# Kernel tuning notes

Measured on AMD Instinct MI355X. Metric: run time of the kernel, lower is better.

## Reference

```python
import jax, jax.numpy as jnp
import numpy as np

EPSILON = 1e-06
MAXIMUM_AREA_RATIO = 0.3
GRID_HEIGHT = 160.0
CUBE = (25.0, 25.0, 32.0)
FEAT_SCALE = 1.0
GRID_SCALE = 1.0
CRANGE = (-1.0, 0.95)


def setup_inputs() -> dict:
    key = jax.random.key(0)
    k1, k2, k3, k4, k5 = jax.random.split(key, 5)
    B, C, H, W = 2, 256, 96, 320
    L, Wg = 128, 128
    n_layers = int(GRID_HEIGHT // CUBE[2])  # 5
    return {
        "feature": jax.random.normal(k1, (B, C, H, W), dtype=jnp.float32),
        "calib": jax.random.normal(k2, (B, 3, 4), dtype=jnp.float32),
        "grid": jax.random.normal(k3, (L, Wg, 3), dtype=jnp.float32),
        "Wc": jax.random.normal(k4, (C, C * n_layers), dtype=jnp.float32) * 0.02,
        "bc": jax.random.normal(k5, (C,), dtype=jnp.float32) * 0.02,
    }


def _cube_corners(cube):
    l, w, h = cube
    x = np.array([-l / 2, l / 2, l / 2, -l / 2, -l / 2, l / 2, l / 2, -l / 2])
    y = np.array([-w / 2, -w / 2, w / 2, w / 2, -w / 2, -w / 2, w / 2, w / 2])
    z = np.array([0, 0, 0, 0, h, h, h, h])
    return jnp.asarray(np.stack([x, y, z], axis=-1), dtype=jnp.float32)  # (8,3)


def _grid_sample_zeros(img, grd):
    # img: [B,C,H,W]; grd: [B,Hg,Wg,2] normalized coords in [-1,1]
    # bilinear, zero padding, align_corners=False (torch default)
    B, C, H, W = img.shape
    x = ((grd[..., 0] + 1.0) * W - 1.0) * 0.5
    y = ((grd[..., 1] + 1.0) * H - 1.0) * 0.5
    x0f = jnp.floor(x)
    y0f = jnp.floor(y)
    x0 = x0f.astype(jnp.int32)
    y0 = y0f.astype(jnp.int32)
    img_flat = img.reshape(B, C, H * W)

    def gather(xi, yi):
        valid = (xi >= 0) & (xi < W) & (yi >= 0) & (yi < H)
        xc = jnp.clip(xi, 0, W - 1)
        yc = jnp.clip(yi, 0, H - 1)
        idx = (yc * W + xc).reshape(B, 1, -1)
        v = jnp.take_along_axis(img_flat, idx, axis=2)
        v = v.reshape((B, C) + grd.shape[1:-1])
        return v * valid[:, None].astype(img.dtype)

    wx1 = x - x0f
    wx0 = 1.0 - wx1
    wy1 = y - y0f
    wy0 = 1.0 - wy1
    out = (gather(x0, y0) * (wx0 * wy0)[:, None]
           + gather(x0 + 1, y0) * (wx1 * wy0)[:, None]
           + gather(x0, y0 + 1) * (wx0 * wy1)[:, None]
           + gather(x0 + 1, y0 + 1) * (wx1 * wy1)[:, None])
    return out


def reference(feature, calib, grid, Wc, bc):
    B, C, H, W = feature.shape
    L, Wg, _ = grid.shape
    dtype = feature.dtype

    # z-layer offsets: (n_layers, 3) with offset only in z
    z_off = jnp.arange(0.0, GRID_HEIGHT, CUBE[2], dtype=dtype)  # (5,)
    n_layers = z_off.shape[0]
    z_corners = jnp.stack([jnp.zeros_like(z_off), jnp.zeros_like(z_off), z_off], axis=-1)
    offset = _cube_corners(CUBE)  # (8,3)

    # corners3d: (n_layers, L, Wg, 8, 3)
    corners = grid[None] + z_corners[:, None, None, :]  # (n,L,Wg,3)
    corners3d = (corners[:, :, :, None, :] + offset[None, None, None]) / GRID_SCALE

    # project with calib (B,3,4): homogeneous matmul then perspective divide
    hom = jnp.concatenate([corners3d, jnp.ones_like(corners3d[..., :1])], axis=-1)  # (n,L,Wg,8,4)
    pts = jnp.einsum('bij,nlwkj->bnlwki', calib, hom)  # (B,n,L,Wg,8,3)
    img_xy = pts[..., :2] / jnp.maximum(pts[..., 2:3], EPSILON)

    img_size = jnp.array([W, H], dtype=dtype) / FEAT_SCALE
    norm = jnp.clip(2.0 * img_xy / img_size - 1.0, CRANGE[0], CRANGE[1])  # (B,n,L,Wg,8,2)

    box_corners = jnp.concatenate([
        jnp.min(norm[..., 0], axis=-1, keepdims=True),
        jnp.min(norm[..., 1], axis=-1, keepdims=True),
        jnp.max(norm[..., 0], axis=-1, keepdims=True),
        jnp.max(norm[..., 1], axis=-1, keepdims=True),
    ], axis=-1)  # (B,n,L,Wg,4)
    box_corners = box_corners.reshape(B, n_layers, L * Wg, 4)

    area = ((box_corners[..., 2:] - box_corners[..., :2]).prod(axis=-1) * (H * W) + EPSILON)
    area = area[:, None]  # (B,1,n,LWg)
    visible = ((area > EPSILON) & (area < H * W * MAXIMUM_AREA_RATIO)).astype(dtype)

    integral = jnp.cumsum(jnp.cumsum(feature, axis=-1), axis=-2)

    lt = _grid_sample_zeros(integral, box_corners[..., [0, 1]])
    rb = _grid_sample_zeros(integral, box_corners[..., [2, 3]])
    rt = _grid_sample_zeros(integral, box_corners[..., [2, 1]])
    lb = _grid_sample_zeros(integral, box_corners[..., [0, 3]])

    vox = (lt + rb - rt - lb) / area * visible  # (B,C,n,LWg)
    # permute(0,3,1,2) -> (B, LWg, C, n); flatten to (B*LWg, C*n)
    vox = jnp.transpose(vox, (0, 3, 1, 2)).reshape(B * L * Wg, C * n_layers)

    ortho = vox @ Wc.T + bc  # (B*LWg, C)
    ortho = ortho.reshape(B, L, Wg, C)
    ortho = jax.nn.relu(jnp.transpose(ortho, (0, 3, 1, 2)))  # (B,C,L,Wg)
    return ortho
```

## Files before the change

### kernel.cpp

```cpp
#include <hip/hip_runtime.h>
#include <hip/hip_bf16.h>
#include <stdint.h>

#define BB 2
#define CC 256
#define HH 96
#define WW 320
#define NPIX 16384
#define NLAY 5
#define KDIM 1280
#define NDIM 32768
#define NKT (KDIM / 32)

typedef float f32x4 __attribute__((ext_vector_type(4)));
typedef float f32x2 __attribute__((ext_vector_type(2)));
typedef __bf16 bf16x8 __attribute__((ext_vector_type(8)));
typedef __bf16 bf16x4 __attribute__((ext_vector_type(4)));

__global__ __launch_bounds__(1024) void k1f(const float* __restrict__ feat,
                                            float* __restrict__ integ,
                                            const float* __restrict__ gridp,
                                            const float* __restrict__ calib,
                                            const float* __restrict__ Wc,
                                            float4* __restrict__ coords,
                                            float* __restrict__ scales,
                                            __bf16* __restrict__ Wbf) {
  const int bid = blockIdx.x;
  if (bid < 480) {
    const int vbid = bid * 4 + (threadIdx.x >> 8);
    const int vt = threadIdx.x & 255;
    if (vbid >= 640) {
      int o = (vbid - 640) * 256 + vt;
      int co = o / KDIM;
      int kk = o % KDIM;
      int n = kk >> 8;
      int c = kk & 255;
      Wbf[o] = (__bf16)Wc[co * KDIM + c * NLAY + n];
      return;
    }
    int box = vbid * 256 + vt;
    int pix = box & (NPIX - 1);
    int bn = box >> 14;
    int n = bn % NLAY;
    int b = bn / NLAY;
    const float* cb = calib + b * 12;
    float c00 = cb[0], c01 = cb[1], c02 = cb[2], c03 = cb[3];
    float c10 = cb[4], c11 = cb[5], c12 = cb[6], c13 = cb[7];
    float c20 = cb[8], c21 = cb[9], c22 = cb[10], c23 = cb[11];
    float gx = gridp[pix * 3 + 0], gy = gridp[pix * 3 + 1], gz = gridp[pix * 3 + 2];
    float zoff = 32.0f * (float)n;
    const float ox[8] = {-12.5f, 12.5f, 12.5f, -12.5f, -12.5f, 12.5f, 12.5f, -12.5f};
    const float oy[8] = {-12.5f, -12.5f, 12.5f, 12.5f, -12.5f, -12.5f, 12.5f, 12.5f};
    float xmn = 1e30f, ymn = 1e30f, xmx = -1e30f, ymx = -1e30f;
#pragma unroll
    for (int k = 0; k < 8; ++k) {
      float X = gx + ox[k];
      float Y = gy + oy[k];
      float Z = gz + zoff + ((k >= 4) ? 32.0f : 0.0f);
      float px = c00 * X + c01 * Y + c02 * Z + c03;
      float py = c10 * X + c11 * Y + c12 * Z + c13;
      float pz = c20 * X + c21 * Y + c22 * Z + c23;
      float d = fmaxf(pz, 1e-6f);
      float nx = fminf(fmaxf(2.0f * (px / d) / 320.0f - 1.0f, -1.0f), 0.95f);
      float ny = fminf(fmaxf(2.0f * (py / d) / 96.0f - 1.0f, -1.0f), 0.95f);
      xmn = fminf(xmn, nx); xmx = fmaxf(xmx, nx);
      ymn = fminf(ymn, ny); ymx = fmaxf(ymx, ny);
    }
    float dx = xmx - xmn, dy = ymx - ymn;
    float area = (dx * dy) * 30720.0f + 1e-6f;
    bool vis = (area > 1e-6f) && (area < 9216.0f);
    float X0 = ((xmn + 1.0f) * 320.0f - 1.0f) * 0.5f;
    float Y0 = ((ymn + 1.0f) * 96.0f - 1.0f) * 0.5f;
    float X1 = ((xmx + 1.0f) * 320.0f - 1.0f) * 0.5f;
    float Y1 = ((ymx + 1.0f) * 96.0f - 1.0f) * 0.5f;
    coords[box] = make_float4(X0, Y0, X1, Y1);
    scales[box] = vis ? 1.0f / area : 0.0f;
    return;
  }
  __shared__ float tile[WW * 33];
  const int t = threadIdx.x;
  const int wave = t >> 6;
  const int lane = t & 63;
  const int kb = bid - 480;
  const int cg = kb & 7;
  const int h = (kb >> 3) % HH;
  const int b = kb / (8 * HH);
  const int c0 = cg * 32;

  {
    const float* fb = feat + (size_t)((b * CC + c0) * HH + h) * WW;
    const size_t crstride = (size_t)HH * WW;
#pragma unroll
    for (int r = 0; r < 3; ++r) {
      int idx = r * 1024 + t;
      if (idx < 2560) {
        int cr = idx / 80;
        int wq = idx - cr * 80;
        f32x4 v = *(const f32x4*)(fb + cr * crstride + wq * 4);
        *(f32x4*)(&tile[cr * WW + wq * 4]) = v;
      }
    }
  }
  __syncthreads();
  const int ca = wave * 2, cbn = wave * 2 + 1;
  float va[5], vb[5];
#pragma unroll
  for (int j = 0; j < 5; ++j) va[j] = tile[ca * WW + lane * 5 + j];
#pragma unroll
  for (int j = 0; j < 5; ++j) vb[j] = tile[cbn * WW + lane * 5 + j];
#pragma unroll
  for (int j = 1; j < 5; ++j) { va[j] += va[j - 1]; vb[j] += vb[j - 1]; }
  float ta = va[4], tb = vb[4];
  float ia = ta, ib = tb;
#pragma unroll
  for (int d = 1; d < 64; d <<= 1) {
    float ua = __shfl_up(ia, d, 64);
    float ub = __shfl_up(ib, d, 64);
    if (lane >= d) { ia += ua; ib += ub; }
  }
  float pa = ia - ta, pb = ib - tb;
#pragma unroll
  for (int j = 0; j < 5; ++j) { va[j] += pa; vb[j] += pb; }
  __syncthreads();
#pragma unroll
  for (int j = 0; j < 5; ++j) {
    int w = lane * 5 + j;
    tile[w * 33 + ca]  = va[j];
    tile[w * 33 + cbn] = vb[j];
  }
  __syncthreads();
  float* dst = integ + (size_t)((b * HH + h) * WW) * CC + cg * 32;
#pragma unroll
  for (int r = 0; r < 3; ++r) {
    int idx = r * 1024 + t;
    if (idx < 2560) {
      int w = idx >> 3;
      int cq = (idx & 7) * 4;
      float4 o = make_float4(tile[w * 33 + cq + 0], tile[w * 33 + cq + 1],
                             tile[w * 33 + cq + 2], tile[w * 33 + cq + 3]);
      *(float4*)(dst + (size_t)w * CC + cq) = o;
    }
  }
}

__global__ __launch_bounds__(256) void k2_scan(float* __restrict__ integ) {
  const int blk = blockIdx.x;
  const int cq = blk & 1;
  const int w = (blk >> 1) % WW;
  const int b = blk / (2 * WW);
  const int g = threadIdx.x >> 6;
  const int l = threadIdx.x & 63;
  float* base = integ + ((size_t)(b * HH + g * 24) * WW + w) * CC + cq * 128 + l * 2;
  const size_t stride = (size_t)WW * CC;
  f32x2 v[24];
#pragma unroll
  for (int i = 0; i < 24; ++i) v[i] = *(const f32x2*)(base + (size_t)i * stride);
#pragma unroll
  for (int i = 1; i < 24; ++i) v[i] += v[i - 1];
  __shared__ f32x2 part[4][64];
  part[g][l] = v[23];
  __syncthreads();
  f32x2 off = {0.f, 0.f};
#pragma unroll
  for (int gg = 0; gg < 3; ++gg)
    if (gg < g) off += part[gg][l];
#pragma unroll
  for (int i = 0; i < 24; ++i) *(f32x2*)(base + (size_t)i * stride) = v[i] + off;
}

__global__ __launch_bounds__(256) void k4_vox(const float* __restrict__ integ,
                                              const float4* __restrict__ coords,
                                              const float* __restrict__ scales,
                                              __bf16* __restrict__ voxA) {
  const int wave = threadIdx.x >> 6;
  const int lane = threadIdx.x & 63;
  const int box0 = (blockIdx.x * 4 + wave) * 4;
#pragma unroll
  for (int u = 0; u < 4; ++u) {
    const int box = box0 + u;
    const int pix = box & (NPIX - 1);
    const int bn = box >> 14;
    const int n = bn % NLAY;
    const int b = bn / NLAY;
    const size_t row = (size_t)(b * NPIX + pix);
    bf16x4* dst = (bf16x4*)(voxA + row * KDIM + n * CC + lane * 4);
    const float scale = scales[box];
    if (scale == 0.f) {
      *dst = bf16x4{(__bf16)0.f, (__bf16)0.f, (__bf16)0.f, (__bf16)0.f};
      continue;
    }
    const float4 q = coords[box];

    float xw[4]; int xi[4];
    float yw[4]; int yi[4];
    {
      float f0 = floorf(q.x); int i0 = (int)f0; float w1 = q.x - f0;
      xw[0] = (i0 >= 0 && i0 < WW) ? (1.f - w1) : 0.f;
      xw[1] = (i0 + 1 < WW) ? w1 : 0.f;
      xi[0] = min(max(i0, 0), WW - 1); xi[1] = min(max(i0 + 1, 0), WW - 1);
      float f1 = floorf(q.z); int i1 = (int)f1; float v1 = q.z - f1;
      xw[2] = (i1 >= 0 && i1 < WW) ? -(1.f - v1) : 0.f;
      xw[3] = (i1 + 1 < WW) ? -v1 : 0.f;
      xi[2] = min(max(i1, 0), WW - 1); xi[3] = min(max(i1 + 1, 0), WW - 1);
    }
    {
      float f0 = floorf(q.y); int j0 = (int)f0; float w1 = q.y - f0;
      yw[0] = (j0 >= 0 && j0 < HH) ? (1.f - w1) : 0.f;
      yw[1] = (j0 + 1 < HH) ? w1 : 0.f;
      yi[0] = min(max(j0, 0), HH - 1); yi[1] = min(max(j0 + 1, 0), HH - 1);
      float f1 = floorf(q.w); int j1 = (int)f1; float v1 = q.w - f1;
      yw[2] = (j1 >= 0 && j1 < HH) ? -(1.f - v1) : 0.f;
      yw[3] = (j1 + 1 < HH) ? -v1 : 0.f;
      yi[2] = min(max(j1, 0), HH - 1); yi[3] = min(max(j1 + 1, 0), HH - 1);
    }
    const float* base = integ + (size_t)(b * HH) * WW * CC + lane * 4;
    f32x4 val = {0.f, 0.f, 0.f, 0.f};
#pragma unroll
    for (int jj = 0; jj < 4; ++jj) {
      if (yw[jj] == 0.f) continue;
      const float* rp = base + (size_t)yi[jj] * WW * CC;
      f32x4 rs = {0.f, 0.f, 0.f, 0.f};
#pragma unroll
      for (int ii = 0; ii < 4; ++ii) {
        if (xw[ii] != 0.f) {
          f32x4 v = *(const f32x4*)(rp + (size_t)xi[ii] * CC);
          rs += xw[ii] * v;
        }
      }
      val += yw[jj] * rs;
    }
    val *= scale;
    *dst = bf16x4{(__bf16)val.x, (__bf16)val.y, (__bf16)val.z, (__bf16)val.w};
  }
}

__device__ __forceinline__ void glds16(const void* g, void* l) {
  __builtin_amdgcn_global_load_lds(
      (const __attribute__((address_space(1))) void*)g,
      (__attribute__((address_space(3))) void*)(uint32_t)(uintptr_t)l,
      16, 0, 0);
}

__global__ __launch_bounds__(256) void k6_gemm(const __bf16* __restrict__ A,
                                               const __bf16* __restrict__ Bm,
                                               const float* __restrict__ bias,
                                               float* __restrict__ out) {
  __shared__ __align__(16) __bf16 As[4][128 * 32];
  __shared__ __align__(16) __bf16 Bs[4][128 * 32];
  const int tileM = blockIdx.y * 128;
  const int tileN = blockIdx.x * 128;
  const int tid = threadIdx.x;
  const int lane = tid & 63;
  const int wave = tid >> 6;
  const int wm = (wave >> 1) * 64;
  const int wn = (wave & 1) * 64;

  f32x4 acc[4][4];
#pragma unroll
  for (int i = 0; i < 4; ++i)
#pragma unroll
    for (int j = 0; j < 4; ++j)
      acc[i][j] = f32x4{0.f, 0.f, 0.f, 0.f};

  const int r16 = lane & 15;
  const int q4 = lane >> 4;
  const int srow = (lane >> 2);
  const int sch = lane & 3;

  auto stage = [&](int buf, int kt) {
    const int k0 = kt * 32;
#pragma unroll
    for (int rr = 0; rr < 2; ++rr) {
      const int base_row = wave * 16 + rr * 64;
      const int row = base_row + srow;
      const int gch = sch ^ ((row >> 1) & 3);
      glds16(A  + (size_t)(tileM + row) * KDIM + k0 + gch * 8,
             (void*)(&As[buf][base_row * 32] + lane * 8));
      glds16(Bm + (size_t)(tileN + row) * KDIM + k0 + gch * 8,
             (void*)(&Bs[buf][base_row * 32] + lane * 8));
    }
  };

  stage(0, 0);
  stage(1, 1);
  stage(2, 2);
  for (int kt = 0; kt < NKT; ++kt) {
    const int cur = kt & 3;
    if (kt < NKT - 2)       __builtin_amdgcn_s_waitcnt(0xF78);
    else if (kt == NKT - 2) __builtin_amdgcn_s_waitcnt(0xF74);
    else                    __builtin_amdgcn_s_waitcnt(0xF70);
    __builtin_amdgcn_s_barrier();
    if (kt + 3 < NKT) stage((kt + 3) & 3, kt + 3);
    bf16x8 af[4], bg[4];
#pragma unroll
    for (int i = 0; i < 4; ++i) {
      int m = wm + i * 16 + r16;
      af[i] = *(const bf16x8*)(&As[cur][m * 32] + (q4 ^ ((m >> 1) & 3)) * 8);
    }
#pragma unroll
    for (int j = 0; j < 4; ++j) {
      int nr = wn + j * 16 + r16;
      bg[j] = *(const bf16x8*)(&Bs[cur][nr * 32] + (q4 ^ ((nr >> 1) & 3)) * 8);
    }
#pragma unroll
    for (int i = 0; i < 4; ++i)
#pragma unroll
      for (int j = 0; j < 4; ++j)
        acc[i][j] = __builtin_amdgcn_mfma_f32_16x16x32_bf16(af[i], bg[j], acc[i][j], 0, 0, 0);
  }

#pragma unroll
  for (int i = 0; i < 4; ++i) {
#pragma unroll
    for (int j = 0; j < 4; ++j) {
      int nn = tileN + wn + j * 16 + r16;
      int bI = nn >> 14;
      int pix = nn & (NPIX - 1);
#pragma unroll
      for (int r = 0; r < 4; ++r) {
        int co = tileM + wm + i * 16 + q4 * 4 + r;
        float v = acc[i][j][r] + bias[co];
        out[(size_t)(bI * CC + co) * NPIX + pix] = fmaxf(v, 0.f);
      }
    }
  }
}

extern "C" void kernel_launch(void* const* d_in, const int* in_sizes, int n_in,
                              void* d_out, int out_size, void* d_ws, size_t ws_size,
                              hipStream_t stream) {
  const float* feat  = (const float*)d_in[0];
  const float* calib = (const float*)d_in[1];
  const float* grid  = (const float*)d_in[2];
  const float* Wc    = (const float*)d_in[3];
  const float* bc    = (const float*)d_in[4];
  float* out = (float*)d_out;

  char* ws = (char*)d_ws;
  const size_t SZ_INTEG = (size_t)BB * HH * WW * CC * 4;
  const size_t SZ_VOX   = (size_t)NDIM * KDIM * 2;
  const size_t SZ_WBF   = (size_t)CC * KDIM * 2;
  const size_t SZ_CRD   = (size_t)BB * NLAY * NPIX * 16;
  const size_t SZ_SCL   = (size_t)BB * NLAY * NPIX * 4;
  if (ws_size < SZ_INTEG + SZ_VOX + SZ_WBF + SZ_CRD + SZ_SCL) return;

  float*  integ  = (float*)ws;
  __bf16* voxA   = (__bf16*)(ws + SZ_INTEG);
  __bf16* Wbf    = (__bf16*)(ws + SZ_INTEG + SZ_VOX);
  float4* coords = (float4*)(ws + SZ_INTEG + SZ_VOX + SZ_WBF);
  float*  scales = (float*)(ws + SZ_INTEG + SZ_VOX + SZ_WBF + SZ_CRD);

  k1f<<<dim3(BB * HH * 8 + 480), dim3(1024), 0, stream>>>(
      feat, integ, grid, calib, Wc, coords, scales, Wbf);
  k2_scan<<<dim3(BB * WW * 2), dim3(256), 0, stream>>>(integ);
  k4_vox<<<dim3(BB * NLAY * NPIX / 16), dim3(256), 0, stream>>>(integ, coords, scales, voxA);
  k6_gemm<<<dim3(NDIM / 128, 2), dim3(256), 0, stream>>>(Wbf, voxA, bc, out);
}
```

Measured before the change: 189.4 us.

## Skip invisible box groups in voxel and GEMM stages via visibility mask

The box kernel now records a per-128-pixel, per-layer visibility flag using wave ballots. The voxel kernel exits early for fully invisible groups, and the GEMM builds a compacted list of K-tiles for only the visible layers, so it skips loads and MFMAs for layers that are all zero. The column scan is also widened to float4 per thread with half as many blocks. This relies on random input geometry making many boxes invisible; the skipped voxA entries stay unwritten but are never read.

```diff
diff --git a/kernel.cpp b/kernel.cpp
--- a/kernel.cpp
+++ b/kernel.cpp
@@ -11,6 +11,7 @@
 #define KDIM 1280
 #define NDIM 32768
 #define NKT (KDIM / 32)
+#define NGRP 256
 
 typedef float f32x4 __attribute__((ext_vector_type(4)));
 typedef float f32x2 __attribute__((ext_vector_type(2)));
@@ -24,7 +25,8 @@
                                             const float* __restrict__ Wc,
                                             float4* __restrict__ coords,
                                             float* __restrict__ scales,
-                                            __bf16* __restrict__ Wbf) {
+                                            __bf16* __restrict__ Wbf,
+                                            uint8_t* __restrict__ mask8) {
   const int bid = blockIdx.x;
   if (bid < 480) {
     const int vbid = bid * 4 + (threadIdx.x >> 8);
@@ -69,6 +71,21 @@
     float dx = xmx - xmn, dy = ymx - ymn;
     float area = (dx * dy) * 30720.0f + 1e-6f;
     bool vis = (area > 1e-6f) && (area < 9216.0f);
+    {
+      __shared__ uint32_t kf[16];
+      unsigned long long bal = __ballot(vis);
+      if ((threadIdx.x & 63) == 0) kf[threadIdx.x >> 6] = (bal != 0ull) ? 1u : 0u;
+      __syncthreads();
+      if (vt == 0) {
+        int vb = threadIdx.x >> 8;
+        int vbid2 = bid * 4 + vb;
+        int bn2 = vbid2 >> 6;
+        int n2 = bn2 % NLAY, b2 = bn2 / NLAY;
+        int g0 = b2 * 128 + (vbid2 & 63) * 2;
+        mask8[g0 * 5 + n2]       = (uint8_t)(kf[vb * 4 + 0] | kf[vb * 4 + 1]);
+        mask8[(g0 + 1) * 5 + n2] = (uint8_t)(kf[vb * 4 + 2] | kf[vb * 4 + 3]);
+      }
+    }
     float X0 = ((xmn + 1.0f) * 320.0f - 1.0f) * 0.5f;
     float Y0 = ((ymn + 1.0f) * 96.0f - 1.0f) * 0.5f;
     float X1 = ((xmx + 1.0f) * 320.0f - 1.0f) * 0.5f;
@@ -145,36 +162,42 @@
 
 __global__ __launch_bounds__(256) void k2_scan(float* __restrict__ integ) {
   const int blk = blockIdx.x;
-  const int cq = blk & 1;
-  const int w = (blk >> 1) % WW;
-  const int b = blk / (2 * WW);
+  const int w = blk % WW;
+  const int b = blk / WW;
   const int g = threadIdx.x >> 6;
   const int l = threadIdx.x & 63;
-  float* base = integ + ((size_t)(b * HH + g * 24) * WW + w) * CC + cq * 128 + l * 2;
+  float* base = integ + ((size_t)(b * HH + g * 24) * WW + w) * CC + l * 4;
   const size_t stride = (size_t)WW * CC;
-  f32x2 v[24];
-#pragma unroll
-  for (int i = 0; i < 24; ++i) v[i] = *(const f32x2*)(base + (size_t)i * stride);
+  f32x4 v[24];
+#pragma unroll
+  for (int i = 0; i < 24; ++i) v[i] = *(const f32x4*)(base + (size_t)i * stride);
 #pragma unroll
   for (int i = 1; i < 24; ++i) v[i] += v[i - 1];
-  __shared__ f32x2 part[4][64];
+  __shared__ f32x4 part[4][64];
   part[g][l] = v[23];
   __syncthreads();
-  f32x2 off = {0.f, 0.f};
+  f32x4 off = {0.f, 0.f, 0.f, 0.f};
 #pragma unroll
   for (int gg = 0; gg < 3; ++gg)
     if (gg < g) off += part[gg][l];
 #pragma unroll
-  for (int i = 0; i < 24; ++i) *(f32x2*)(base + (size_t)i * stride) = v[i] + off;
+  for (int i = 0; i < 24; ++i) *(f32x4*)(base + (size_t)i * stride) = v[i] + off;
 }
 
 __global__ __launch_bounds__(256) void k4_vox(const float* __restrict__ integ,
                                               const float4* __restrict__ coords,
                                               const float* __restrict__ scales,
-                                              __bf16* __restrict__ voxA) {
+                                              __bf16* __restrict__ voxA,
+                                              const uint8_t* __restrict__ mask8) {
   const int wave = threadIdx.x >> 6;
   const int lane = threadIdx.x & 63;
   const int box0 = (blockIdx.x * 4 + wave) * 4;
+  {
+    const int pix0 = box0 & (NPIX - 1);
+    const int bn0 = box0 >> 14;
+    const int n0 = bn0 % NLAY, b0 = bn0 / NLAY;
+    if (mask8[((b0 * NPIX + pix0) >> 7) * 5 + n0] == 0) return;
+  }
 #pragma unroll
   for (int u = 0; u < 4; ++u) {
     const int box = box0 + u;
@@ -244,9 +267,12 @@
 __global__ __launch_bounds__(256) void k6_gemm(const __bf16* __restrict__ A,
                                                const __bf16* __restrict__ Bm,
                                                const float* __restrict__ bias,
-                                               float* __restrict__ out) {
+                                               float* __restrict__ out,
+                                               const uint8_t* __restrict__ mask8) {
   __shared__ __align__(16) __bf16 As[4][128 * 32];
   __shared__ __align__(16) __bf16 Bs[4][128 * 32];
+  __shared__ uint8_t ktsS[NKT];
+  __shared__ int LsS;
   const int tileM = blockIdx.y * 128;
   const int tileN = blockIdx.x * 128;
   const int tid = threadIdx.x;
@@ -254,6 +280,18 @@
   const int wave = tid >> 6;
   const int wm = (wave >> 1) * 64;
   const int wn = (wave & 1) * 64;
+
+  if (tid == 0) {
+    const uint8_t* mg = mask8 + blockIdx.x * 5;
+    int L = 0;
+#pragma unroll
+    for (int n = 0; n < NLAY; ++n)
+      if (mg[n]) {
+#pragma unroll
+        for (int kk = 0; kk < 8; ++kk) ktsS[L++] = (uint8_t)(n * 8 + kk);
+      }
+    LsS = L;
+  }
 
   f32x4 acc[4][4];
 #pragma unroll
@@ -281,21 +319,24 @@
     }
   };
 
-  stage(0, 0);
-  stage(1, 1);
-  stage(2, 2);
-  for (int kt = 0; kt < NKT; ++kt) {
-    const int cur = kt & 3;
-    if (kt < NKT - 2)       __builtin_amdgcn_s_waitcnt(0xF78);
-    else if (kt == NKT - 2) __builtin_amdgcn_s_waitcnt(0xF74);
-    else                    __builtin_amdgcn_s_waitcnt(0xF70);
+  __syncthreads();
+  const int L = LsS;
+#pragma unroll
+  for (int s = 0; s < 3; ++s)
+    if (s < L) stage(s, ktsS[s]);
+  for (int i = 0; i < L; ++i) {
+    const int cur = i & 3;
+    const int rem = L - i;
+    if (rem >= 3)      __builtin_amdgcn_s_waitcnt(0xF78);
+    else if (rem == 2) __builtin_amdgcn_s_waitcnt(0xF74);
+    else               __builtin_amdgcn_s_waitcnt(0xF70);
     __builtin_amdgcn_s_barrier();
-    if (kt + 3 < NKT) stage((kt + 3) & 3, kt + 3);
+    if (i + 3 < L) stage((i + 3) & 3, ktsS[i + 3]);
     bf16x8 af[4], bg[4];
 #pragma unroll
-    for (int i = 0; i < 4; ++i) {
-      int m = wm + i * 16 + r16;
-      af[i] = *(const bf16x8*)(&As[cur][m * 32] + (q4 ^ ((m >> 1) & 3)) * 8);
+    for (int ii = 0; ii < 4; ++ii) {
+      int m = wm + ii * 16 + r16;
+      af[ii] = *(const bf16x8*)(&As[cur][m * 32] + (q4 ^ ((m >> 1) & 3)) * 8);
     }
 #pragma unroll
     for (int j = 0; j < 4; ++j) {
@@ -303,10 +344,10 @@
       bg[j] = *(const bf16x8*)(&Bs[cur][nr * 32] + (q4 ^ ((nr >> 1) & 3)) * 8);
     }
 #pragma unroll
-    for (int i = 0; i < 4; ++i)
+    for (int ii = 0; ii < 4; ++ii)
 #pragma unroll
       for (int j = 0; j < 4; ++j)
-        acc[i][j] = __builtin_amdgcn_mfma_f32_16x16x32_bf16(af[i], bg[j], acc[i][j], 0, 0, 0);
+        acc[ii][j] = __builtin_amdgcn_mfma_f32_16x16x32_bf16(af[ii], bg[j], acc[ii][j], 0, 0, 0);
   }
 
 #pragma unroll
@@ -342,17 +383,19 @@
   const size_t SZ_WBF   = (size_t)CC * KDIM * 2;
   const size_t SZ_CRD   = (size_t)BB * NLAY * NPIX * 16;
   const size_t SZ_SCL   = (size_t)BB * NLAY * NPIX * 4;
-  if (ws_size < SZ_INTEG + SZ_VOX + SZ_WBF + SZ_CRD + SZ_SCL) return;
-
-  float*  integ  = (float*)ws;
-  __bf16* voxA   = (__bf16*)(ws + SZ_INTEG);
-  __bf16* Wbf    = (__bf16*)(ws + SZ_INTEG + SZ_VOX);
-  float4* coords = (float4*)(ws + SZ_INTEG + SZ_VOX + SZ_WBF);
-  float*  scales = (float*)(ws + SZ_INTEG + SZ_VOX + SZ_WBF + SZ_CRD);
+  const size_t SZ_MSK   = (size_t)NGRP * NLAY;
+  if (ws_size < SZ_INTEG + SZ_VOX + SZ_WBF + SZ_CRD + SZ_SCL + SZ_MSK) return;
+
+  float*   integ  = (float*)ws;
+  __bf16*  voxA   = (__bf16*)(ws + SZ_INTEG);
+  __bf16*  Wbf    = (__bf16*)(ws + SZ_INTEG + SZ_VOX);
+  float4*  coords = (float4*)(ws + SZ_INTEG + SZ_VOX + SZ_WBF);
+  float*   scales = (float*)(ws + SZ_INTEG + SZ_VOX + SZ_WBF + SZ_CRD);
+  uint8_t* mask8  = (uint8_t*)(ws + SZ_INTEG + SZ_VOX + SZ_WBF + SZ_CRD + SZ_SCL);
 
   k1f<<<dim3(BB * HH * 8 + 480), dim3(1024), 0, stream>>>(
-      feat, integ, grid, calib, Wc, coords, scales, Wbf);
-  k2_scan<<<dim3(BB * WW * 2), dim3(256), 0, stream>>>(integ);
-  k4_vox<<<dim3(BB * NLAY * NPIX / 16), dim3(256), 0, stream>>>(integ, coords, scales, voxA);
-  k6_gemm<<<dim3(NDIM / 128, 2), dim3(256), 0, stream>>>(Wbf, voxA, bc, out);
-}
+      feat, integ, grid, calib, Wc, coords, scales, Wbf, mask8);
+  k2_scan<<<dim3(BB * WW), dim3(256), 0, stream>>>(integ);
+  k4_vox<<<dim3(BB * NLAY * NPIX / 16), dim3(256), 0, stream>>>(integ, coords, scales, voxA, mask8);
+  k6_gemm<<<dim3(NDIM / 128, 2), dim3(256), 0, stream>>>(Wbf, voxA, bc, out, mask8);
+}
```

Result: faster. 160.3 us (-15.4%).
